# Kernel optimization log

Hardware: AMD Instinct MI355X
Metric: run time of the kernel (lower is better)

Reference implementation:

```python
import jax, jax.numpy as jnp
import numpy as np
import itertools

# ---- static config (mirrors args in init_kwargs) ----
BS = 4                        # num_processes
H, W = 480, 640               # frame_height, frame_width
NC = 16                       # num_sem_categories
C = 4 + NC                    # obs channels: RGB + depth + semantics
RES = 5                       # map_resolution (cm per cell)
ZRES = 5
MAP_CM = 4800 // 2            # map_size_cm // global_downscaling
M = MAP_CM // RES             # 480 local-map cells
VR = 100                      # vision_range
FOV = 79.0                    # hfov (deg)
DU = 1                        # du_scale
AGENT_H = 1.55 * 100.0        # camera_height * 100 (cm)
MAXH = int(360 / ZRES)        # 72
MINH = int(-40 / ZRES)        # -8
ZH = MAXH - MINH              # 80 height bins
MAP_THR, EXP_THR, CAT_THR = 1.0, 1.0, 5.0
DEG = 57.29577951308232
MIN_Z = int(5 / ZRES - MINH)                    # 9
MAX_Z = int((AGENT_H + 1 + 50) / ZRES - MINH)   # 49
XCAM = (W - 1.0) / 2.0
ZCAM = (H - 1.0) / 2.0
FOC = (W / 2.0) / np.tan(np.deg2rad(FOV / 2.0))


def _splat_feat_nd(feat, coords, grid_dims):
    # feat: (B,F,N) ; coords: (B,3,N) normalized to [-1,1] ; trilinear scatter-add
    B, Fc, N = feat.shape
    G = grid_dims[0] * grid_dims[1] * grid_dims[2]
    grid_flat = jnp.zeros((B, Fc, G), feat.dtype)
    pos_dim, wts_dim = [], []
    for d in range(3):
        gd = grid_dims[d]
        pos = coords[:, d, :] * (gd / 2.0) + gd / 2.0   # (B,N) voxel-space coord
        fl = jnp.floor(pos)
        pd, wd = [], []
        for ix in (0.0, 1.0):
            pos_ix = fl + ix
            safe = ((pos_ix > 0) & (pos_ix < gd)).astype(feat.dtype)
            wd.append((1.0 - jnp.abs(pos - pos_ix)) * safe)
            pd.append(pos_ix * safe)  # unsafe points dumped at index 0 with weight 0
        pos_dim.append(pd)
        wts_dim.append(wd)
    for ix_d in itertools.product((0, 1), (0, 1), (0, 1)):
        w = wts_dim[0][ix_d[0]] * wts_dim[1][ix_d[1]] * wts_dim[2][ix_d[2]]
        idx = jnp.zeros_like(w)
        for d in range(3):
            idx = idx * grid_dims[d] + pos_dim[d][ix_d[d]]
        idx = idx.astype(jnp.int32)                     # (B,N)
        vals = feat * w[:, None, :]                     # (B,F,N)
        grid_flat = jax.vmap(lambda g, i, v: g.at[:, i].add(v))(grid_flat, idx, vals)
    grid_flat = jnp.round(grid_flat)
    return grid_flat.reshape((B, Fc) + tuple(grid_dims))


def _affine_grid(theta, Hh, Ww):
    # align_corners=True base grid
    xs = jnp.linspace(-1.0, 1.0, Ww)
    ys = jnp.linspace(-1.0, 1.0, Hh)
    Xg, Yg = jnp.meshgrid(xs, ys)
    base = jnp.stack([Xg, Yg, jnp.ones_like(Xg)], -1)   # (H,W,3)
    return jnp.einsum('bij,hwj->bhwi', theta, base)     # (B,H,W,2)


def _grid_sample(img, grid):
    # bilinear, align_corners=True, zero padding; img (B,C,H,W), grid (B,Ho,Wo,2)
    B, Cc, Hh, Ww = img.shape
    x = (grid[..., 0] + 1.0) * 0.5 * (Ww - 1)
    y = (grid[..., 1] + 1.0) * 0.5 * (Hh - 1)
    x0 = jnp.floor(x)
    y0 = jnp.floor(y)
    wx1 = x - x0
    wy1 = y - y0

    def gather(ix, iy):
        valid = ((ix >= 0) & (ix <= Ww - 1) & (iy >= 0) & (iy <= Hh - 1)).astype(img.dtype)
        ixc = jnp.clip(ix, 0, Ww - 1).astype(jnp.int32)
        iyc = jnp.clip(iy, 0, Hh - 1).astype(jnp.int32)
        v = jax.vmap(lambda im, yy, xx: im[:, yy, xx])(img, iyc, ixc)  # (B,C,Ho,Wo)
        return v * valid[:, None]

    return (gather(x0, y0) * ((1 - wx1) * (1 - wy1))[:, None]
            + gather(x0 + 1, y0) * (wx1 * (1 - wy1))[:, None]
            + gather(x0, y0 + 1) * ((1 - wx1) * wy1)[:, None]
            + gather(x0 + 1, y0 + 1) * (wx1 * wy1)[:, None])


def _forward(obs, pose_obs, maps_last, poses_last, view_angles):
    bs = obs.shape[0]
    depth = obs[:, 3, ::DU, ::DU]                        # (B,h,w) depth in cm
    gx = jnp.arange(W, dtype=obs.dtype)[None, None, ::DU]
    gz = jnp.arange(H - 1, -1, -1, dtype=obs.dtype)[None, ::DU, None]
    Xp = (gx - XCAM) * depth / FOC
    Zp = (gz - ZCAM) * depth / FOC
    # rotate about x-axis by per-env view angle (deg), then lift by agent height
    a = jnp.deg2rad(view_angles)[:, None, None]
    ca, sa = jnp.cos(a), jnp.sin(a)
    Xv = Xp
    Yv = ca * depth - sa * Zp
    Zv = sa * depth + ca * Zp + AGENT_H
    # shift_loc rotation angle is pi/2 - pi/2 = 0 -> identity rot, only x shift
    Xv = Xv + VR * RES / 2.0
    # normalize to [-1,1] voxel coords
    xs = (Xv / RES - VR // 2.0) / VR * 2.0
    ys = (Yv / RES - VR // 2.0) / VR * 2.0
    zs = (Zv / ZRES - (MAXH + MINH) // 2.0) / (MAXH - MINH) * 2.0
    coords = jnp.stack([xs, ys, zs], 1).reshape(bs, 3, -1)   # (B,3,N)
    # features: channel 0 = ones (occupancy), rest = avg-pooled semantic masks
    sem = obs[:, 4:]
    pooled = sem.reshape(bs, NC, H // DU, DU, W // DU, DU).mean((3, 5))
    N = (H // DU) * (W // DU)
    feat = jnp.concatenate([jnp.ones((bs, 1, N), obs.dtype), pooled.reshape(bs, NC, N)], 1)
    voxels = _splat_feat_nd(feat, coords, (VR, VR, ZH)).swapaxes(2, 3)  # (B,1+NC,VR,VR,ZH)
    agg = voxels[..., MIN_Z:MAX_Z].sum(4)
    fp_map_pred = jnp.clip(agg[:, :1] / MAP_THR, 0.0, 1.0)
    fp_exp_pred = jnp.clip(voxels.sum(4)[:, :1] / EXP_THR, 0.0, 1.0)
    cat_pred = jnp.clip(agg[:, 1:] / CAT_THR, 0.0, 1.0)
    agent_view = jnp.zeros((bs, C, M, M), obs.dtype)
    x1 = M // 2 - VR // 2
    x2 = x1 + VR
    y1 = M // 2
    y2 = y1 + VR
    agent_view = agent_view.at[:, 0:1, y1:y2, x1:x2].set(fp_map_pred)
    agent_view = agent_view.at[:, 1:2, y1:y2, x1:x2].set(fp_exp_pred)
    agent_view = agent_view.at[:, 4:, y1:y2, x1:x2].set(cat_pred)
    # pose integration (get_new_pose_batch, note sequential in-place semantics)
    o = poses_last[:, 2] / DEG
    yy = poses_last[:, 1] + pose_obs[:, 0] * jnp.sin(o) + pose_obs[:, 1] * jnp.cos(o)
    xx = poses_last[:, 0] + pose_obs[:, 0] * jnp.cos(o) - pose_obs[:, 1] * jnp.sin(o)
    tt = poses_last[:, 2] + pose_obs[:, 2] * DEG
    tt = jnp.fmod(tt - 180.0, 360.0) + 180.0
    tt = jnp.fmod(tt + 180.0, 360.0) - 180.0
    current_poses = jnp.stack([xx, yy, tt], 1)
    # st_pose is detached in the original
    st = jax.lax.stop_gradient(current_poses)
    half = M // 2
    stx = -(st[:, 0] * 100.0 / RES - half) / half
    sty = -(st[:, 1] * 100.0 / RES - half) / half
    t = (90.0 - st[:, 2]) * np.pi / 180.0
    ct, s_t = jnp.cos(t), jnp.sin(t)
    zero, one = jnp.zeros_like(ct), jnp.ones_like(ct)
    theta1 = jnp.stack([jnp.stack([ct, -s_t, zero], 1), jnp.stack([s_t, ct, zero], 1)], 1)
    theta2 = jnp.stack([jnp.stack([one, zero, stx], 1), jnp.stack([zero, one, sty], 1)], 1)
    rotated = _grid_sample(agent_view, _affine_grid(theta1, M, M))
    translated = _grid_sample(rotated, _affine_grid(theta2, M, M))
    map_pred = jnp.maximum(maps_last, translated)
    # pose_pred aliases the in-place-updated poses_last in torch == current_poses
    return fp_map_pred, map_pred, current_poses, current_poses, translated


def setup_inputs() -> dict:
    key = jax.random.key(0)
    k1, k2, k3, k4 = jax.random.split(key, 4)
    obs = jax.random.uniform(k1, (BS, C, H, W), jnp.float32)
    obs = obs.at[:, 3].multiply(400.0)  # depth channel in cm, up to 4 m
    pose_obs = jax.random.uniform(k2, (BS, 3), jnp.float32) * 0.25
    maps_last = jax.random.uniform(k3, (BS, C, M, M), jnp.float32)
    poses_last = jax.random.uniform(k4, (BS, 3), jnp.float32)
    view_angles = jnp.zeros((BS,), jnp.float32)
    return {"obs": obs, "pose_obs": pose_obs, "maps_last": maps_last,
            "poses_last": poses_last, "view_angles": view_angles}


def reference(obs, pose_obs, maps_last, poses_last, view_angles):
    return _forward(obs, pose_obs, maps_last, poses_last, view_angles)
```

## Files before the change

kernel.cpp:

```cpp
#include <hip/hip_runtime.h>
#include <math.h>

#define BS 4
#define HH 480
#define WW 640
#define NPX (HH * WW)
#define NC 16
#define CHN 20
#define MM 480
#define VRD 100
#define ZHD 80
#define MINZ 9
#define MAXZ 49
#define CAP 8192

#define OFF0 0
#define OFF1 40000
#define OFF2 18472000
#define OFF3 18472012
#define OFF4 18472024
#define OFFM 28840000
#define OFFR 29560000
#define OFFC 36113600

__device__ __forceinline__ void pix2pos(int w, int h, float depth, float ca, float sa,
                                        float foc, float& px, float& py, float& pz) {
    float gx = (float)w;
    float gz = (float)(HH - 1 - h);
    float Xp = (gx - 319.5f) * depth / foc;
    float Zp = (gz - 239.5f) * depth / foc;
    float Yv = ca * depth - sa * Zp;
    float Zv = sa * depth + ca * Zp + 155.0f;
    float Xv = Xp + 250.0f;
    float xs = (Xv / 5.0f - 50.0f) / 100.0f * 2.0f;
    float ys = (Yv / 5.0f - 50.0f) / 100.0f * 2.0f;
    float zs = (Zv / 5.0f - 32.0f) / 80.0f * 2.0f;
    px = xs * 50.0f + 50.0f;
    py = ys * 50.0f + 50.0f;
    pz = zs * 40.0f + 40.0f;
}

__global__ __launch_bounds__(256) void bin_kernel(const float* __restrict__ obs,
                                                  const float* __restrict__ va,
                                                  int* __restrict__ cnt,
                                                  float2* __restrict__ rec,
                                                  float foc) {
    int idx = blockIdx.x * blockDim.x + threadIdx.x;
    if (idx >= BS * NPX) return;
    int b   = idx / NPX;
    int rem = idx % NPX;
    float depth = obs[((size_t)b * CHN + 3) * NPX + rem];
    int h = rem / WW, w = rem % WW;
    float a  = va[b] * 0.017453292519943295f;
    float ca = cosf(a), sa = sinf(a);
    float px, py, pz;
    pix2pos(w, h, depth, ca, sa, foc, px, py, pz);
    int f = (int)floorf(py);
    if (f < 0 || f > 99) return;
    int slot = atomicAdd(cnt + (b * VRD + f) * 16, 1);
    if (slot < CAP) {
        float2 r; r.x = __int_as_float(rem); r.y = depth;
        rec[(size_t)(b * VRD + f) * CAP + slot] = r;
    }
}

__global__ __launch_bounds__(256) void slice_v0_kernel(const int* __restrict__ cnt,
                                                       const float2* __restrict__ rec,
                                                       const float* __restrict__ va,
                                                       float* __restrict__ maps,
                                                       float* __restrict__ out0,
                                                       float foc) {
    __shared__ float acc[VRD * ZHD];
    int s = blockIdx.x;
    int b = blockIdx.y;
    int tid = threadIdx.x;
    for (int i = tid; i < VRD * ZHD; i += 256) acc[i] = 0.0f;
    __syncthreads();

    float a  = va[b] * 0.017453292519943295f;
    float ca = cosf(a), sa = sinf(a);
    int sm1 = (s > 0) ? s - 1 : 0;
    int n0 = (s > 0) ? min(cnt[(b * VRD + sm1) * 16], CAP) : 0;
    int n1 = min(cnt[(b * VRD + s) * 16], CAP);
    const float2* r0 = rec + (size_t)(b * VRD + sm1) * CAP;
    const float2* r1 = rec + (size_t)(b * VRD + s) * CAP;
    int N = n0 + n1;
    float fs = (float)s;

    for (int t = tid; t < N; t += 256) {
        float2 rv = (t < n0) ? r0[t] : r1[t - n0];
        int rem = __float_as_int(rv.x);
        float depth = rv.y;
        float px, py, pz;
        pix2pos(rem % WW, rem / WW, depth, ca, sa, foc, px, py, pz);
        float wy = 1.0f - fabsf(py - fs);
        if (s == 0 || wy <= 0.0f) continue;
        float fx = floorf(px), fz = floorf(pz);
        #pragma unroll
        for (int i = 0; i < 2; i++) {
            float cxp = fx + (float)i;
            if (!(cxp > 0.0f && cxp < 100.0f)) continue;
            float wxv = 1.0f - fabsf(px - cxp);
            int xi = (int)cxp;
            #pragma unroll
            for (int k = 0; k < 2; k++) {
                float czp = fz + (float)k;
                if (!(czp > 0.0f && czp < 80.0f)) continue;
                float wzv = 1.0f - fabsf(pz - czp);
                float wv = wy * wxv * wzv;
                if (wv != 0.0f) atomicAdd(&acc[xi * ZHD + (int)czp], wv);
            }
        }
    }
    __syncthreads();

    if (tid < VRD) {
        float s_all = 0.0f, s_agg = 0.0f;
        #pragma unroll 4
        for (int z = 0; z < ZHD; z++) {
            float r = rintf(acc[tid * ZHD + z]);
            s_all += r;
            if (z >= MINZ && z < MAXZ) s_agg += r;
        }
        float fm = fminf(fmaxf(s_agg, 0.0f), 1.0f);
        float fe = fminf(fmaxf(s_all, 0.0f), 1.0f);
        maps[((size_t)(b * 18 + 0) * VRD + s) * VRD + tid] = fm;
        maps[((size_t)(b * 18 + 1) * VRD + s) * VRD + tid] = fe;
        out0[((size_t)b * VRD + s) * VRD + tid] = fm;
    }
}

__global__ __launch_bounds__(256, 5) void slice_vc_kernel(const float* __restrict__ obs,
                                                          const int* __restrict__ cnt,
                                                          const float2* __restrict__ rec,
                                                          const float* __restrict__ va,
                                                          float* __restrict__ maps,
                                                          float foc) {
    __shared__ float acc[40 * VRD * 2];
    int bid  = blockIdx.x;
    int wgid = (bid & 7) * 400 + (bid >> 3);
    int s  = wgid % VRD;
    int p  = wgid / VRD;
    int b  = p & 3;
    int cg = p >> 2;
    int tid = threadIdx.x;
    for (int i = tid; i < 40 * VRD * 2; i += 256) acc[i] = 0.0f;
    __syncthreads();

    float a  = va[b] * 0.017453292519943295f;
    float ca = cosf(a), sa = sinf(a);
    int sm1 = (s > 0) ? s - 1 : 0;
    int n0 = (s > 0) ? min(cnt[(b * VRD + sm1) * 16], CAP) : 0;
    int n1 = min(cnt[(b * VRD + s) * 16], CAP);
    const float2* r0 = rec + (size_t)(b * VRD + sm1) * CAP;
    const float2* r1 = rec + (size_t)(b * VRD + s) * CAP;
    int N = (s == 0) ? 0 : n0 + n1;
    float fs = (float)s;
    const float* sb = obs + ((size_t)b * CHN + 4 + cg * 2) * NPX;

    for (int t = tid; t < N; t += 256) {
        float2 rv = (t < n0) ? r0[t] : r1[t - n0];
        int rem = __float_as_int(rv.x);
        float depth = rv.y;
        float px, py, pz;
        pix2pos(rem % WW, rem / WW, depth, ca, sa, foc, px, py, pz);
        float wy = 1.0f - fabsf(py - fs);
        if (wy <= 0.0f) continue;
        if (pz < 8.0f || pz >= 49.0f) continue;
        float fx = floorf(px);
        float fz = floorf(pz);
        bool xv0 = (fx > 0.0f && fx < 100.0f);
        bool xv1 = (fx + 1.0f > 0.0f && fx + 1.0f < 100.0f);
        if (!xv0 && !xv1) continue;
        float s0 = sb[rem];
        float s1 = sb[rem + NPX];
        #pragma unroll
        for (int i2 = 0; i2 < 2; i2++) {
            float cxp = fx + (float)i2;
            if (!(cxp > 0.0f && cxp < 100.0f)) continue;
            float wxy = wy * (1.0f - fabsf(px - cxp));
            int xi = (int)cxp;
            #pragma unroll
            for (int k = 0; k < 2; k++) {
                float czp = fz + (float)k;
                if (czp < 9.0f || czp > 48.0f) continue;
                float w3 = wxy * (1.0f - fabsf(pz - czp));
                if (w3 == 0.0f) continue;
                float* dst = &acc[(((int)czp - MINZ) * VRD + xi) * 2];
                atomicAdd(dst + 0, w3 * s0);
                atomicAdd(dst + 1, w3 * s1);
            }
        }
    }
    __syncthreads();

    for (int i = tid; i < VRD * 2; i += 256) {
        int x = i >> 1, c = i & 1;
        float ssum = 0.0f;
        #pragma unroll 4
        for (int z = 0; z < 40; z++)
            ssum += rintf(acc[(z * VRD + x) * 2 + c]);
        float v = fminf(fmaxf(ssum * 0.2f, 0.0f), 1.0f);
        maps[((size_t)(b * 18 + 2 + cg * 2 + c) * VRD + s) * VRD + x] = v;
    }
}

__device__ __forceinline__ void pose_params(const float* __restrict__ pose_obs,
                                            const float* __restrict__ poses_last,
                                            int b, float& ct, float& st,
                                            float& stx, float& sty) {
    const float DEG = 57.29577951308232f;
    float o  = poses_last[b*3+2] / DEG;
    float so = sinf(o), co = cosf(o);
    float yy = poses_last[b*3+1] + pose_obs[b*3+0]*so + pose_obs[b*3+1]*co;
    float xx = poses_last[b*3+0] + pose_obs[b*3+0]*co - pose_obs[b*3+1]*so;
    float tt = poses_last[b*3+2] + pose_obs[b*3+2]*DEG;
    tt = fmodf(tt - 180.0f, 360.0f) + 180.0f;
    tt = fmodf(tt + 180.0f, 360.0f) - 180.0f;
    stx = -((xx*100.0f/5.0f) - 240.0f) / 240.0f;
    sty = -((yy*100.0f/5.0f) - 240.0f) / 240.0f;
    float t = (90.0f - tt) * 0.017453292519943295f;
    ct = cosf(t); st = sinf(t);
}

__global__ __launch_bounds__(64) void pose_kernel(const float* __restrict__ pose_obs,
                                                  const float* __restrict__ poses_last,
                                                  float* __restrict__ out) {
    int b = threadIdx.x;
    if (b >= BS) return;
    const float DEG = 57.29577951308232f;
    float o  = poses_last[b*3+2] / DEG;
    float so = sinf(o), co = cosf(o);
    float yy = poses_last[b*3+1] + pose_obs[b*3+0]*so + pose_obs[b*3+1]*co;
    float xx = poses_last[b*3+0] + pose_obs[b*3+0]*co - pose_obs[b*3+1]*so;
    float tt = poses_last[b*3+2] + pose_obs[b*3+2]*DEG;
    tt = fmodf(tt - 180.0f, 360.0f) + 180.0f;
    tt = fmodf(tt + 180.0f, 360.0f) - 180.0f;
    out[OFF2 + b*3+0] = xx; out[OFF2 + b*3+1] = yy; out[OFF2 + b*3+2] = tt;
    out[OFF3 + b*3+0] = xx; out[OFF3 + b*3+1] = yy; out[OFF3 + b*3+2] = tt;
}

__global__ __launch_bounds__(256) void rotate_kernel(const float* __restrict__ maps,
                                                     const float* __restrict__ pose_obs,
                                                     const float* __restrict__ poses_last,
                                                     float* __restrict__ rot) {
    int idx = blockIdx.x * blockDim.x + threadIdx.x;
    if (idx >= BS * MM * MM) return;
    int b   = idx / (MM * MM);
    int rem = idx % (MM * MM);
    int y   = rem / MM;
    int x   = rem % MM;
    float ct, st, stx, sty;
    pose_params(pose_obs, poses_last, b, ct, st, stx, sty);
    float Xg = -1.0f + (float)x * (2.0f / 479.0f);
    float Yg = -1.0f + (float)y * (2.0f / 479.0f);
    float gx = ct * Xg - st * Yg;
    float gy = st * Xg + ct * Yg;
    float xf = (gx + 1.0f) * 0.5f * 479.0f;
    float yf = (gy + 1.0f) * 0.5f * 479.0f;
    float x0 = floorf(xf), y0 = floorf(yf);
    float fx = xf - x0, fy = yf - y0;
    float cw[4] = {(1.0f - fx) * (1.0f - fy), fx * (1.0f - fy),
                   (1.0f - fx) * fy,          fx * fy};
    float cx[4] = {x0, x0 + 1.0f, x0, x0 + 1.0f};
    float cy[4] = {y0, y0, y0 + 1.0f, y0 + 1.0f};
    float acc[18];
    #pragma unroll
    for (int m = 0; m < 18; m++) acc[m] = 0.0f;
    #pragma unroll
    for (int k = 0; k < 4; k++) {
        float fxk = cx[k], fyk = cy[k];
        if (!(fxk >= 0.0f && fxk <= 479.0f && fyk >= 0.0f && fyk <= 479.0f)) continue;
        int ix = (int)fxk, iy = (int)fyk;
        if (iy < 240 || iy >= 340 || ix < 190 || ix >= 290) continue;
        int mi = iy - 240, mj = ix - 190;
        float w = cw[k];
        const float* mp = maps + (size_t)b * 18 * VRD * VRD + mi * VRD + mj;
        #pragma unroll
        for (int m = 0; m < 18; m++) acc[m] += w * mp[(size_t)m * VRD * VRD];
    }
    size_t obase = ((size_t)b * CHN) * MM * MM + (size_t)y * MM + x;
    rot[obase + (size_t)0 * MM * MM] = acc[0];
    rot[obase + (size_t)1 * MM * MM] = acc[1];
    rot[obase + (size_t)2 * MM * MM] = 0.0f;
    rot[obase + (size_t)3 * MM * MM] = 0.0f;
    #pragma unroll
    for (int m = 2; m < 18; m++)
        rot[obase + (size_t)(m + 2) * MM * MM] = acc[m];
}

__global__ __launch_bounds__(256) void translate_kernel(const float* __restrict__ rot,
                                                        const float* __restrict__ pose_obs,
                                                        const float* __restrict__ poses_last,
                                                        float* __restrict__ tr) {
    int idx = blockIdx.x * blockDim.x + threadIdx.x;
    if (idx >= BS * MM * MM) return;
    int b   = idx / (MM * MM);
    int rem = idx % (MM * MM);
    int y   = rem / MM;
    int x   = rem % MM;
    float ct, st, stx, sty;
    pose_params(pose_obs, poses_last, b, ct, st, stx, sty);
    float Xg = -1.0f + (float)x * (2.0f / 479.0f);
    float Yg = -1.0f + (float)y * (2.0f / 479.0f);
    float xf = (Xg + stx + 1.0f) * 0.5f * 479.0f;
    float yf = (Yg + sty + 1.0f) * 0.5f * 479.0f;
    float x0 = floorf(xf), y0 = floorf(yf);
    float fx = xf - x0, fy = yf - y0;
    float cw[4] = {(1.0f - fx) * (1.0f - fy), fx * (1.0f - fy),
                   (1.0f - fx) * fy,          fx * fy};
    float cxs[4] = {x0, x0 + 1.0f, x0, x0 + 1.0f};
    float cys[4] = {y0, y0, y0 + 1.0f, y0 + 1.0f};
    bool vk[4]; int offk[4];
    #pragma unroll
    for (int k = 0; k < 4; k++) {
        vk[k] = (cxs[k] >= 0.0f && cxs[k] <= 479.0f && cys[k] >= 0.0f && cys[k] <= 479.0f);
        offk[k] = vk[k] ? ((int)cys[k] * MM + (int)cxs[k]) : 0;
    }
    #pragma unroll
    for (int c = 0; c < CHN; c++) {
        const float* rp = rot + ((size_t)b * CHN + c) * MM * MM;
        float v = 0.0f;
        #pragma unroll
        for (int k = 0; k < 4; k++)
            if (vk[k]) v += cw[k] * rp[offk[k]];
        tr[((size_t)b * CHN + c) * MM * MM + (size_t)y * MM + x] = v;
    }
}

__global__ __launch_bounds__(256) void max_kernel(const float* __restrict__ maps_last,
                                                  const float* __restrict__ tr,
                                                  float* __restrict__ mp) {
    int i = blockIdx.x * blockDim.x + threadIdx.x;
    int n4 = BS * CHN * MM * MM / 4;
    if (i >= n4) return;
    float4 a = ((const float4*)maps_last)[i];
    float4 t = ((const float4*)tr)[i];
    float4 r;
    r.x = fmaxf(a.x, t.x);
    r.y = fmaxf(a.y, t.y);
    r.z = fmaxf(a.z, t.z);
    r.w = fmaxf(a.w, t.w);
    ((float4*)mp)[i] = r;
}

extern "C" void kernel_launch(void* const* d_in, const int* in_sizes, int n_in,
                              void* d_out, int out_size, void* d_ws, size_t ws_size,
                              hipStream_t stream) {
    const float* obs         = (const float*)d_in[0];
    const float* pose_obs    = (const float*)d_in[1];
    const float* maps_last   = (const float*)d_in[2];
    const float* poses_last  = (const float*)d_in[3];
    const float* view_angles = (const float*)d_in[4];
    float* out = (float*)d_out;

    float*  maps = out + OFFM;
    float2* rec  = (float2*)(out + OFFR);
    int*    cnt  = (int*)(out + OFFC);

    hipMemsetAsync(cnt, 0, 400 * 16 * sizeof(int), stream);

    const float foc = (float)(320.0 / tan(39.5 * M_PI / 180.0));

    int npix = BS * NPX;
    bin_kernel<<<(npix + 255) / 256, 256, 0, stream>>>(obs, view_angles, cnt, rec, foc);

    dim3 sgrid(VRD, BS);
    slice_v0_kernel<<<sgrid, 256, 0, stream>>>(cnt, rec, view_angles, maps, out + OFF0, foc);
    slice_vc_kernel<<<dim3(VRD * BS * 8), 256, 0, stream>>>(obs, cnt, rec, view_angles,
                                                            maps, foc);

    pose_kernel<<<1, 64, 0, stream>>>(pose_obs, poses_last, out);

    int nmap = BS * MM * MM;
    rotate_kernel<<<(nmap + 255) / 256, 256, 0, stream>>>(maps, pose_obs, poses_last,
                                                          out + OFF1);
    translate_kernel<<<(nmap + 255) / 256, 256, 0, stream>>>(out + OFF1, pose_obs,
                                                             poses_last, out + OFF4);
    int n4 = BS * CHN * MM * MM / 4;
    max_kernel<<<(n4 + 255) / 256, 256, 0, stream>>>(maps_last, out + OFF4, out + OFF1);
}
```

Baseline: 1.263 ms.

## Store precomputed voxel coords in bins and merge slice kernels into one split-channel grid

The bin kernel now stores the projected px,py,pz plus the pixel index as a float4, so slice kernels no longer recompute the projection. The two slice kernels become one kernel over 18 channel groups per slice: one semantic channel per block, plus two blocks that split the occupancy height range and combine partial sums through global atomics and a fixup kernel. Each thread processes four records at a time so gathers can be issued together, and occupancy is raised through smaller shared arrays. In exchange the record traffic doubles, the out buffer is reused as scratch at a new offset, and there is an extra kernel launch.

```diff
diff --git a/kernel.cpp b/kernel.cpp
--- a/kernel.cpp
+++ b/kernel.cpp
@@ -20,8 +20,9 @@
 #define OFF3 18472012
 #define OFF4 18472024
 #define OFFM 28840000
-#define OFFR 29560000
 #define OFFC 36113600
+#define OFFS 36120000
+#define GEO  40000
 
 __device__ __forceinline__ void pix2pos(int w, int h, float depth, float ca, float sa,
                                         float foc, float& px, float& py, float& pz) {
@@ -43,7 +44,7 @@
 __global__ __launch_bounds__(256) void bin_kernel(const float* __restrict__ obs,
                                                   const float* __restrict__ va,
                                                   int* __restrict__ cnt,
-                                                  float2* __restrict__ rec,
+                                                  float4* __restrict__ geo,
                                                   float foc) {
     int idx = blockIdx.x * blockDim.x + threadIdx.x;
     if (idx >= BS * NPX) return;
@@ -59,150 +60,129 @@
     if (f < 0 || f > 99) return;
     int slot = atomicAdd(cnt + (b * VRD + f) * 16, 1);
     if (slot < CAP) {
-        float2 r; r.x = __int_as_float(rem); r.y = depth;
-        rec[(size_t)(b * VRD + f) * CAP + slot] = r;
-    }
-}
-
-__global__ __launch_bounds__(256) void slice_v0_kernel(const int* __restrict__ cnt,
-                                                       const float2* __restrict__ rec,
-                                                       const float* __restrict__ va,
+        float4 r;
+        r.x = px; r.y = py; r.z = pz; r.w = __int_as_float(rem);
+        geo[(size_t)(b * VRD + f) * CAP + slot] = r;
+    }
+}
+
+__global__ __launch_bounds__(256, 6) void slice_kernel(const float* __restrict__ obs,
+                                                       const int* __restrict__ cnt,
+                                                       const float4* __restrict__ geo,
                                                        float* __restrict__ maps,
-                                                       float* __restrict__ out0,
-                                                       float foc) {
-    __shared__ float acc[VRD * ZHD];
-    int s = blockIdx.x;
-    int b = blockIdx.y;
+                                                       float* __restrict__ stage) {
+    __shared__ float acc[40 * VRD];
+    int bid  = blockIdx.x;
+    int wgid = (bid & 7) * 900 + (bid >> 3);
+    int s  = wgid % VRD;
+    int p  = wgid / VRD;
+    int b  = p & 3;
+    int c  = p >> 2;
     int tid = threadIdx.x;
-    for (int i = tid; i < VRD * ZHD; i += 256) acc[i] = 0.0f;
+    for (int i = tid; i < 40 * VRD; i += 256) acc[i] = 0.0f;
     __syncthreads();
 
-    float a  = va[b] * 0.017453292519943295f;
-    float ca = cosf(a), sa = sinf(a);
+    bool isocc = (c >= 16);
+    float clo   = isocc ? ((c == 16) ? 1.0f : 40.0f) : 9.0f;
+    float chi   = isocc ? ((c == 16) ? 40.0f : 80.0f) : 49.0f;
+    int   zbase = isocc ? ((c == 16) ? 0 : 40) : 9;
+    const float* sb = isocc ? (const float*)0 : obs + ((size_t)b * CHN + 4 + c) * NPX;
+
     int sm1 = (s > 0) ? s - 1 : 0;
     int n0 = (s > 0) ? min(cnt[(b * VRD + sm1) * 16], CAP) : 0;
     int n1 = min(cnt[(b * VRD + s) * 16], CAP);
-    const float2* r0 = rec + (size_t)(b * VRD + sm1) * CAP;
-    const float2* r1 = rec + (size_t)(b * VRD + s) * CAP;
-    int N = n0 + n1;
-    float fs = (float)s;
-
-    for (int t = tid; t < N; t += 256) {
-        float2 rv = (t < n0) ? r0[t] : r1[t - n0];
-        int rem = __float_as_int(rv.x);
-        float depth = rv.y;
-        float px, py, pz;
-        pix2pos(rem % WW, rem / WW, depth, ca, sa, foc, px, py, pz);
-        float wy = 1.0f - fabsf(py - fs);
-        if (s == 0 || wy <= 0.0f) continue;
-        float fx = floorf(px), fz = floorf(pz);
-        #pragma unroll
-        for (int i = 0; i < 2; i++) {
-            float cxp = fx + (float)i;
-            if (!(cxp > 0.0f && cxp < 100.0f)) continue;
-            float wxv = 1.0f - fabsf(px - cxp);
-            int xi = (int)cxp;
-            #pragma unroll
-            for (int k = 0; k < 2; k++) {
-                float czp = fz + (float)k;
-                if (!(czp > 0.0f && czp < 80.0f)) continue;
-                float wzv = 1.0f - fabsf(pz - czp);
-                float wv = wy * wxv * wzv;
-                if (wv != 0.0f) atomicAdd(&acc[xi * ZHD + (int)czp], wv);
-            }
-        }
-    }
-    __syncthreads();
-
-    if (tid < VRD) {
-        float s_all = 0.0f, s_agg = 0.0f;
-        #pragma unroll 4
-        for (int z = 0; z < ZHD; z++) {
-            float r = rintf(acc[tid * ZHD + z]);
-            s_all += r;
-            if (z >= MINZ && z < MAXZ) s_agg += r;
-        }
-        float fm = fminf(fmaxf(s_agg, 0.0f), 1.0f);
-        float fe = fminf(fmaxf(s_all, 0.0f), 1.0f);
-        maps[((size_t)(b * 18 + 0) * VRD + s) * VRD + tid] = fm;
-        maps[((size_t)(b * 18 + 1) * VRD + s) * VRD + tid] = fe;
-        out0[((size_t)b * VRD + s) * VRD + tid] = fm;
-    }
-}
-
-__global__ __launch_bounds__(256, 5) void slice_vc_kernel(const float* __restrict__ obs,
-                                                          const int* __restrict__ cnt,
-                                                          const float2* __restrict__ rec,
-                                                          const float* __restrict__ va,
-                                                          float* __restrict__ maps,
-                                                          float foc) {
-    __shared__ float acc[40 * VRD * 2];
-    int bid  = blockIdx.x;
-    int wgid = (bid & 7) * 400 + (bid >> 3);
-    int s  = wgid % VRD;
-    int p  = wgid / VRD;
-    int b  = p & 3;
-    int cg = p >> 2;
-    int tid = threadIdx.x;
-    for (int i = tid; i < 40 * VRD * 2; i += 256) acc[i] = 0.0f;
-    __syncthreads();
-
-    float a  = va[b] * 0.017453292519943295f;
-    float ca = cosf(a), sa = sinf(a);
-    int sm1 = (s > 0) ? s - 1 : 0;
-    int n0 = (s > 0) ? min(cnt[(b * VRD + sm1) * 16], CAP) : 0;
-    int n1 = min(cnt[(b * VRD + s) * 16], CAP);
-    const float2* r0 = rec + (size_t)(b * VRD + sm1) * CAP;
-    const float2* r1 = rec + (size_t)(b * VRD + s) * CAP;
+    const float4* g0 = geo + (size_t)(b * VRD + sm1) * CAP;
+    const float4* g1 = geo + (size_t)(b * VRD + s) * CAP;
     int N = (s == 0) ? 0 : n0 + n1;
     float fs = (float)s;
-    const float* sb = obs + ((size_t)b * CHN + 4 + cg * 2) * NPX;
-
-    for (int t = tid; t < N; t += 256) {
-        float2 rv = (t < n0) ? r0[t] : r1[t - n0];
-        int rem = __float_as_int(rv.x);
-        float depth = rv.y;
-        float px, py, pz;
-        pix2pos(rem % WW, rem / WW, depth, ca, sa, foc, px, py, pz);
-        float wy = 1.0f - fabsf(py - fs);
-        if (wy <= 0.0f) continue;
-        if (pz < 8.0f || pz >= 49.0f) continue;
-        float fx = floorf(px);
-        float fz = floorf(pz);
-        bool xv0 = (fx > 0.0f && fx < 100.0f);
-        bool xv1 = (fx + 1.0f > 0.0f && fx + 1.0f < 100.0f);
-        if (!xv0 && !xv1) continue;
-        float s0 = sb[rem];
-        float s1 = sb[rem + NPX];
-        #pragma unroll
-        for (int i2 = 0; i2 < 2; i2++) {
-            float cxp = fx + (float)i2;
-            if (!(cxp > 0.0f && cxp < 100.0f)) continue;
-            float wxy = wy * (1.0f - fabsf(px - cxp));
-            int xi = (int)cxp;
+
+    for (int base = tid * 4; base < N; base += 1024) {
+        float4 g[4];
+        #pragma unroll
+        for (int j = 0; j < 4; j++) {
+            int t = base + j;
+            g[j] = (t < N) ? ((t < n0) ? g0[t] : g1[t - n0])
+                           : make_float4(0.0f, -10.0f, 0.0f, 0.0f);
+        }
+        bool act[4];
+        #pragma unroll
+        for (int j = 0; j < 4; j++) {
+            float wy = 1.0f - fabsf(g[j].y - fs);
+            bool ok = (wy > 0.0f);
+            ok = ok && (g[j].z > clo - 1.0f) && (g[j].z < chi);
+            float fx = floorf(g[j].x);
+            ok = ok && (fx + 1.0f > 0.0f) && (fx < 100.0f);
+            act[j] = ok;
+        }
+        float sv[4];
+        #pragma unroll
+        for (int j = 0; j < 4; j++)
+            sv[j] = (!isocc && act[j]) ? sb[__float_as_int(g[j].w)] : 1.0f;
+        #pragma unroll
+        for (int j = 0; j < 4; j++) {
+            if (!act[j]) continue;
+            float px = g[j].x, pz = g[j].z;
+            float wy = 1.0f - fabsf(g[j].y - fs);
+            float fx = floorf(px), fz = floorf(pz);
             #pragma unroll
-            for (int k = 0; k < 2; k++) {
-                float czp = fz + (float)k;
-                if (czp < 9.0f || czp > 48.0f) continue;
-                float w3 = wxy * (1.0f - fabsf(pz - czp));
-                if (w3 == 0.0f) continue;
-                float* dst = &acc[(((int)czp - MINZ) * VRD + xi) * 2];
-                atomicAdd(dst + 0, w3 * s0);
-                atomicAdd(dst + 1, w3 * s1);
+            for (int i2 = 0; i2 < 2; i2++) {
+                float cxp = fx + (float)i2;
+                if (!(cxp > 0.0f && cxp < 100.0f)) continue;
+                float wxy = wy * (1.0f - fabsf(px - cxp));
+                int xi = (int)cxp;
+                #pragma unroll
+                for (int k = 0; k < 2; k++) {
+                    float czp = fz + (float)k;
+                    if (czp < clo || czp >= chi) continue;
+                    float w3 = wxy * (1.0f - fabsf(pz - czp));
+                    if (w3 == 0.0f) continue;
+                    atomicAdd(&acc[((int)czp - zbase) * VRD + xi], w3 * sv[j]);
+                }
             }
         }
     }
     __syncthreads();
 
-    for (int i = tid; i < VRD * 2; i += 256) {
-        int x = i >> 1, c = i & 1;
-        float ssum = 0.0f;
-        #pragma unroll 4
-        for (int z = 0; z < 40; z++)
-            ssum += rintf(acc[(z * VRD + x) * 2 + c]);
-        float v = fminf(fmaxf(ssum * 0.2f, 0.0f), 1.0f);
-        maps[((size_t)(b * 18 + 2 + cg * 2 + c) * VRD + s) * VRD + x] = v;
-    }
+    if (!isocc) {
+        for (int x = tid; x < VRD; x += 256) {
+            float ssum = 0.0f;
+            #pragma unroll 8
+            for (int z = 0; z < 40; z++) ssum += rintf(acc[z * VRD + x]);
+            maps[((size_t)(b * 18 + 2 + c) * VRD + s) * VRD + x] =
+                fminf(fmaxf(ssum * 0.2f, 0.0f), 1.0f);
+        }
+    } else {
+        int cell0 = (c == 16) ? 0 : 40;
+        for (int x = tid; x < VRD; x += 256) {
+            float s_all = 0.0f, s_agg = 0.0f;
+            #pragma unroll 8
+            for (int z = 0; z < 40; z++) {
+                float r = rintf(acc[z * VRD + x]);
+                s_all += r;
+                int cell = cell0 + z;
+                if (cell >= MINZ && cell < MAXZ) s_agg += r;
+            }
+            int o = (b * VRD + s) * VRD + x;
+            atomicAdd(stage + o, s_all);
+            atomicAdd(stage + 40000 + o, s_agg);
+        }
+    }
+}
+
+__global__ __launch_bounds__(256) void fixup_kernel(const float* __restrict__ stage,
+                                                    float* __restrict__ maps,
+                                                    float* __restrict__ out0) {
+    int idx = blockIdx.x * blockDim.x + threadIdx.x;
+    if (idx >= BS * VRD * VRD) return;
+    int b = idx / (VRD * VRD);
+    int r = idx % (VRD * VRD);
+    float all = stage[idx];
+    float agg = stage[40000 + idx];
+    float fm = fminf(fmaxf(agg, 0.0f), 1.0f);
+    float fe = fminf(fmaxf(all, 0.0f), 1.0f);
+    maps[(size_t)(b * 18 + 0) * 10000 + r] = fm;
+    maps[(size_t)(b * 18 + 1) * 10000 + r] = fe;
+    out0[idx] = fm;
 }
 
 __device__ __forceinline__ void pose_params(const float* __restrict__ pose_obs,
@@ -354,21 +334,21 @@
     const float* view_angles = (const float*)d_in[4];
     float* out = (float*)d_out;
 
-    float*  maps = out + OFFM;
-    float2* rec  = (float2*)(out + OFFR);
-    int*    cnt  = (int*)(out + OFFC);
-
-    hipMemsetAsync(cnt, 0, 400 * 16 * sizeof(int), stream);
+    float*  maps  = out + OFFM;
+    float4* geo   = (float4*)(out + GEO);
+    int*    cnt   = (int*)(out + OFFC);
+    float*  stage = out + OFFS;
+
+    hipMemsetAsync(cnt, 0, (6400 + 80000) * sizeof(float), stream);
 
     const float foc = (float)(320.0 / tan(39.5 * M_PI / 180.0));
 
     int npix = BS * NPX;
-    bin_kernel<<<(npix + 255) / 256, 256, 0, stream>>>(obs, view_angles, cnt, rec, foc);
-
-    dim3 sgrid(VRD, BS);
-    slice_v0_kernel<<<sgrid, 256, 0, stream>>>(cnt, rec, view_angles, maps, out + OFF0, foc);
-    slice_vc_kernel<<<dim3(VRD * BS * 8), 256, 0, stream>>>(obs, cnt, rec, view_angles,
-                                                            maps, foc);
+    bin_kernel<<<(npix + 255) / 256, 256, 0, stream>>>(obs, view_angles, cnt, geo, foc);
+
+    slice_kernel<<<dim3(VRD * BS * 18), 256, 0, stream>>>(obs, cnt, geo, maps, stage);
+
+    fixup_kernel<<<(BS * VRD * VRD + 255) / 256, 256, 0, stream>>>(stage, maps, out + OFF0);
 
     pose_kernel<<<1, 64, 0, stream>>>(pose_obs, poses_last, out);
 
```

Measured after the change: 1.237 ms. 1.02x faster.
